# Kernel tuning notes

Measured on AMD Instinct MI355X. Metric: run time of the kernel, lower is better.

## Reference

```python
import jax, jax.numpy as jnp
import numpy as np

B, L, D, Y = 8, 2500, 512, 8921

def setup_inputs() -> dict:
    key = jax.random.key(0)
    k1, k2, k3, k4 = jax.random.split(key, 4)
    x = jax.random.normal(k1, (B, L, D), dtype=jnp.float32)
    # xavier-ish init scale for the label-attention and output matrices
    scale = (2.0 / (Y + D)) ** 0.5
    U_w = jax.random.normal(k2, (Y, D), dtype=jnp.float32) * scale
    final_w = jax.random.normal(k3, (Y, D), dtype=jnp.float32) * scale
    final_b = jax.random.normal(k4, (Y,), dtype=jnp.float32) * 0.01
    return {"x": x, "U_w": U_w, "final_w": final_w, "final_b": final_b}

def reference(x, U_w, final_w, final_b):
    # scores[b, y, l] = U_w[y, :] . x[b, l, :]
    scores = jnp.einsum('yd,bld->byl', U_w, x)            # (B, Y, L)
    alpha = jax.nn.softmax(scores, axis=2)                 # softmax over seq dim
    m = jnp.einsum('byl,bld->byd', alpha, x)               # (B, Y, D)
    y = jnp.einsum('yd,byd->by', final_w, m) + final_b     # (B, Y)
    return y
```

## Files before the change

kernel.cpp:

```cpp
#include <hip/hip_runtime.h>
#include <hip/hip_bf16.h>

#define NB 8
#define NL 2500
#define ND 512
#define NY 8921

#define BM 256
#define BN 256
#define BK 32
#define NKS 16
#define LPAD 2560
#define NLT 10
#define NYB 70
#define YPAD 8960

#define SPLIT 5
#define LSPL_MAIN 2

#define TILE 16384
#define GT_BYTES ((size_t)NYB * NKS * TILE)
#define XT_BYTES ((size_t)NB * NLT * NKS * TILE)
#define P_ELEMS  ((size_t)SPLIT * NB * YPAD)
#define P_BYTES  (P_ELEMS * 4)

typedef short s8v __attribute__((ext_vector_type(8)));
typedef float f4v __attribute__((ext_vector_type(4)));

__device__ __forceinline__ unsigned short f2bf(float f) {
  unsigned int u = __float_as_uint(f);
  return (unsigned short)((u + 0x7FFFu + ((u >> 16) & 1u)) >> 16);
}
__device__ __forceinline__ unsigned int pk2(float a, float b) {
  return (unsigned int)f2bf(a) | ((unsigned int)f2bf(b) << 16);
}
__device__ __forceinline__ void async_copy16(const char* g, char* l) {
  __builtin_amdgcn_global_load_lds(
      (const __attribute__((address_space(1))) void*)g,
      (__attribute__((address_space(3))) void*)l, 16, 0, 0);
}

__device__ __forceinline__ int tile_off(int r, int gn) {
  int rp = r >> 1;
  return rp * 128 + ((((r & 1) << 6) | (gn << 4)) ^ ((rp & 7) << 4));
}

__global__ void cvt_g_kernel(const float* __restrict__ U, const float* __restrict__ W,
                             char* __restrict__ Gt) {
  int c = blockIdx.x * 256 + threadIdx.x;
  int g10 = c & 1023;
  int tile = c >> 10;
  int ks = tile & 15, yblk = tile >> 4;
  int r = g10 >> 2, gn = g10 & 3;
  int rg = yblk * 256 + r;
  int y = rg >> 1;
  uint4 o;
  if (y < NY) {
    const float* src = (rg & 1) ? W : U;
    const float4* p = (const float4*)(src + (size_t)y * ND + ks * BK + gn * 8);
    float4 f0 = p[0], f1 = p[1];
    o.x = pk2(f0.x, f0.y); o.y = pk2(f0.z, f0.w);
    o.z = pk2(f1.x, f1.y); o.w = pk2(f1.z, f1.w);
  } else {
    o = make_uint4(0u, 0u, 0u, 0u);
  }
  *(uint4*)(Gt + (size_t)tile * TILE + tile_off(r, gn)) = o;
}

__global__ void cvt_x_kernel(const float* __restrict__ x, char* __restrict__ Xt) {
  int c = blockIdx.x * 256 + threadIdx.x;
  int g10 = c & 1023;
  int tile = c >> 10;
  int ks = tile & 15, rest = tile >> 4;
  int t = rest % NLT, b = rest / NLT;
  int r = g10 >> 2, gn = g10 & 3;
  int l = t * 256 + r;
  uint4 o;
  if (l < NL) {
    const float4* p = (const float4*)(x + ((size_t)b * NL + l) * ND + ks * BK + gn * 8);
    float4 f0 = p[0], f1 = p[1];
    o.x = pk2(f0.x, f0.y); o.y = pk2(f0.z, f0.w);
    o.z = pk2(f1.x, f1.y); o.w = pk2(f1.z, f1.w);
  } else {
    o = make_uint4(0u, 0u, 0u, 0u);
  }
  *(uint4*)(Xt + (size_t)tile * TILE + tile_off(r, gn)) = o;
}

template<int LSPL, int NSPL, bool PARTIAL>
__global__ __launch_bounds__(512, 2) void fused_kernel(
    const char* __restrict__ Gt, const char* __restrict__ Xt,
    const float* __restrict__ bias, float* __restrict__ out,
    float* __restrict__ PD, float* __restrict__ PN)
{
  __shared__ uint4 ring[8192];
  char* ringC = (char*)ring;

  constexpr int NS = LSPL * NKS;

  const int tid  = threadIdx.x;
  const int lane = tid & 63;
  const int w    = tid >> 6;
  const int wr   = w >> 2;
  const int wc   = w & 3;
  const int cl   = lane & 15, g = lane >> 4;

  const int id    = blockIdx.x;
  const int bb    = id & 7;
  const int n     = id >> 3;
  const int yblk  = n / NSPL;
  const int split = n - yblk * NSPL;
  const int tbase = split * LSPL;

  const char* GA = Gt + (size_t)yblk * NKS * TILE;
  const char* XB = Xt + ((size_t)bb * NLT + tbase) * NKS * TILE;

  f4v acc[8][4];
  float runD[8][2], runN[8][2];
  #pragma unroll
  for (int mi = 0; mi < 8; ++mi)
    #pragma unroll
    for (int p = 0; p < 2; ++p) { runD[mi][p] = 0.f; runN[mi][p] = 0.f; }

  int aoff[8], boff[4];
  #pragma unroll
  for (int j = 0; j < 8; ++j) aoff[j] = tile_off(wr * 128 + j * 16 + cl, g);
  #pragma unroll
  for (int ni = 0; ni < 4; ++ni) boff[ni] = tile_off(wc * 64 + ni * 16 + cl, g);

  const int t16 = tid << 4;
  auto stageA = [&](int s) {
    const char* ga = GA + (size_t)(s & 15) * TILE;
    char* la = ringC + (s & 3) * TILE + (w << 10);
    async_copy16(ga + t16, la);
    async_copy16(ga + 8192 + t16, la + 8192);
  };
  auto stageB = [&](int s) {
    const char* gb = XB + (size_t)s * TILE;
    char* lb = ringC + 65536 + (s & 3) * TILE + (w << 10);
    async_copy16(gb + t16, lb);
    async_copy16(gb + 8192 + t16, lb + 8192);
  };

  stageA(0); stageB(0);
  stageA(1); stageB(1);
  stageA(2); stageB(2);
  asm volatile("s_waitcnt vmcnt(4)" ::: "memory");
  __builtin_amdgcn_s_barrier();
  asm volatile("" ::: "memory");

  s8v bvA[4], afA[4], bvB[4], afB[4], a47[4];
  {
    const char* A0 = ringC;
    const char* B0 = ringC + 65536;
    #pragma unroll
    for (int ni = 0; ni < 4; ++ni) bvA[ni] = *(const s8v*)(B0 + boff[ni]);
    #pragma unroll
    for (int j = 0; j < 4; ++j)    afA[j] = *(const s8v*)(A0 + aoff[j]);
  }

#define K_STEP(U, CBV, CAF, NBV, NAF)                                          \
  do {                                                                         \
    const int u_  = (U);                                                       \
    const int ks_ = u_ & (NKS - 1);                                            \
    const char* A_ = ringC + (u_ & 3) * TILE;                                  \
    if (ks_ == 0) {                                                            \
      _Pragma("unroll")                                                        \
      for (int mi = 0; mi < 8; ++mi)                                           \
        _Pragma("unroll")                                                      \
        for (int ni = 0; ni < 4; ++ni)                                         \
          _Pragma("unroll")                                                    \
          for (int q = 0; q < 4; ++q) acc[mi][ni][q] = 0.f;                    \
    }                                                                          \
    if (u_ + 3 < NS) { stageA(u_ + 3); stageB(u_ + 3); }                       \
    _Pragma("unroll")                                                          \
    for (int j = 0; j < 4; ++j) a47[j] = *(const s8v*)(A_ + aoff[4 + j]);      \
    __builtin_amdgcn_sched_barrier(0);                                         \
    __builtin_amdgcn_s_setprio(1);                                             \
    _Pragma("unroll")                                                          \
    for (int j = 0; j < 4; ++j)                                                \
      _Pragma("unroll")                                                        \
      for (int ni = 0; ni < 4; ++ni)                                           \
        acc[j][ni] = __builtin_amdgcn_mfma_f32_16x16x32_bf16(                  \
            CAF[j], CBV[ni], acc[j][ni], 0, 0, 0);                             \
    __builtin_amdgcn_s_setprio(0);                                             \
    __builtin_amdgcn_sched_barrier(0);                                         \
    if (u_ + 1 < NS) {                                                         \
      const char* An_ = ringC + ((u_ + 1) & 3) * TILE;                         \
      const char* Bn_ = ringC + 65536 + ((u_ + 1) & 3) * TILE;                 \
      _Pragma("unroll")                                                        \
      for (int ni = 0; ni < 4; ++ni) NBV[ni] = *(const s8v*)(Bn_ + boff[ni]);  \
      _Pragma("unroll")                                                        \
      for (int j = 0; j < 4; ++j)    NAF[j] = *(const s8v*)(An_ + aoff[j]);    \
    }                                                                          \
    __builtin_amdgcn_sched_barrier(0);                                         \
    __builtin_amdgcn_s_setprio(1);                                             \
    _Pragma("unroll")                                                          \
    for (int j = 0; j < 4; ++j)                                                \
      _Pragma("unroll")                                                        \
      for (int ni = 0; ni < 4; ++ni)                                           \
        acc[4 + j][ni] = __builtin_amdgcn_mfma_f32_16x16x32_bf16(              \
            a47[j], CBV[ni], acc[4 + j][ni], 0, 0, 0);                         \
    __builtin_amdgcn_s_setprio(0);                                             \
    if (ks_ == NKS - 1) {                                                      \
      const int lbase = (tbase + (u_ >> 4)) * BN + wc * 64 + cl;               \
      _Pragma("unroll")                                                        \
      for (int mi = 0; mi < 8; ++mi) {                                         \
        _Pragma("unroll")                                                      \
        for (int p = 0; p < 2; ++p) {                                          \
          float se = 0.f, ste = 0.f;                                           \
          _Pragma("unroll")                                                    \
          for (int ni = 0; ni < 4; ++ni) {                                     \
            bool valid = (lbase + ni * 16) < NL;                               \
            float sv = valid ? acc[mi][ni][2 * p] : -1e30f;                    \
            float e = __expf(sv);                                              \
            se += e;                                                           \
            ste += e * acc[mi][ni][2 * p + 1];                                 \
          }                                                                    \
          runD[mi][p] += se;                                                   \
          runN[mi][p] += ste;                                                  \
        }                                                                      \
      }                                                                        \
    }                                                                          \
    if (u_ <= NS - 4) {                                                        \
      asm volatile("s_waitcnt vmcnt(4)" ::: "memory");                         \
    } else if (u_ == NS - 3) {                                                 \
      asm volatile("s_waitcnt vmcnt(0)" ::: "memory");                         \
    }                                                                          \
    __builtin_amdgcn_s_barrier();                                              \
    asm volatile("" ::: "memory");                                             \
  } while (0)

  for (int uu = 0; uu < NS; uu += 2) {
    K_STEP(uu,     bvA, afA, bvB, afB);
    K_STEP(uu + 1, bvB, afB, bvA, afA);
  }
#undef K_STEP

  #pragma unroll
  for (int mi = 0; mi < 8; ++mi)
    #pragma unroll
    for (int p = 0; p < 2; ++p) {
      float d = runD[mi][p], nn = runN[mi][p];
      #pragma unroll
      for (int off = 1; off < 16; off <<= 1) {
        d += __shfl_xor(d, off);
        nn += __shfl_xor(nn, off);
      }
      runD[mi][p] = d; runN[mi][p] = nn;
    }

  __syncthreads();
  float* sm = (float*)ring;
  if (cl == 0) {
    #pragma unroll
    for (int mi = 0; mi < 8; ++mi)
      #pragma unroll
      for (int p = 0; p < 2; ++p) {
        int lab = wr * 64 + mi * 8 + 2 * g + p;
        float* s2 = sm + (lab * 4 + wc) * 2;
        s2[0] = runD[mi][p]; s2[1] = runN[mi][p];
      }
  }
  __syncthreads();
  if (tid < 128) {
    float D = 0.f, N = 0.f;
    #pragma unroll
    for (int q = 0; q < 4; ++q) {
      const float* s2 = sm + (tid * 4 + q) * 2;
      D += s2[0]; N += s2[1];
    }
    int y = yblk * 128 + tid;
    if constexpr (PARTIAL) {
      size_t o = ((size_t)split * NB + bb) * YPAD + y;
      PD[o] = D; PN[o] = N;
    } else {
      if (y < NY) out[(size_t)bb * NY + y] = N / D + bias[y];
    }
  }
}

__global__ void merge_kernel(const float* __restrict__ PD, const float* __restrict__ PN,
                             const float* __restrict__ bias, float* __restrict__ out) {
  int idx = blockIdx.x * 256 + threadIdx.x;
  int b = idx / YPAD, y = idx - b * YPAD;
  if (y >= NY) return;
  float D = 0.f, N = 0.f;
  #pragma unroll
  for (int s = 0; s < SPLIT; ++s) {
    size_t o = ((size_t)s * NB + b) * YPAD + y;
    D += PD[o];
    N += PN[o];
  }
  out[(size_t)b * NY + y] = N / D + bias[y];
}

extern "C" void kernel_launch(void* const* d_in, const int* in_sizes, int n_in,
                              void* d_out, int out_size, void* d_ws, size_t ws_size,
                              hipStream_t stream) {
  const float* xf   = (const float*)d_in[0];
  const float* Uf   = (const float*)d_in[1];
  const float* Wf   = (const float*)d_in[2];
  const float* bias = (const float*)d_in[3];
  float* out = (float*)d_out;

  char* Gt = (char*)d_ws;
  char* Xt = Gt + GT_BYTES;
  float* PD = (float*)(Xt + XT_BYTES);
  float* PN = PD + P_ELEMS;

  cvt_g_kernel<<<4480, 256, 0, stream>>>(Uf, Wf, Gt);
  cvt_x_kernel<<<5120, 256, 0, stream>>>(xf, Xt);

  const size_t need_main = GT_BYTES + XT_BYTES + 2 * P_BYTES;
  if (ws_size >= need_main) {
    fused_kernel<LSPL_MAIN, SPLIT, true><<<NYB * NB * SPLIT, 512, 0, stream>>>(
        Gt, Xt, bias, out, PD, PN);
    merge_kernel<<<NB * YPAD / 256, 256, 0, stream>>>(PD, PN, bias, out);
  } else {
    fused_kernel<NLT, 1, false><<<NYB * NB, 512, 0, stream>>>(
        Gt, Xt, bias, out, PD, PN);
  }
}
```

Baseline: 375.6 us.

## Load X fragments directly from global and shrink LDS ring to double buffer

The X conversion kernel now writes a fragment-major layout, so each wave can load its MFMA B fragments straight from global memory into registers instead of staging them through LDS. The LDS ring is cut from four A+B stages (128KB) to two A-only stages (32KB). The prefetch distance drops to one step with a full vmcnt(0) wait each iteration, and A fragments are read from LDS within the step rather than prefetched. The smaller LDS footprint may allow more blocks per CU. The cost is shallower latency hiding, and each B fragment is now fetched from global by two waves instead of once per block.

```diff
diff --git a/kernel.cpp b/kernel.cpp
--- a/kernel.cpp
+++ b/kernel.cpp
@@ -19,8 +19,9 @@
 #define LSPL_MAIN 2
 
 #define TILE 16384
+#define XSTEP 16384
 #define GT_BYTES ((size_t)NYB * NKS * TILE)
-#define XT_BYTES ((size_t)NB * NLT * NKS * TILE)
+#define XT_BYTES ((size_t)NB * NLT * NKS * XSTEP)
 #define P_ELEMS  ((size_t)SPLIT * NB * YPAD)
 #define P_BYTES  (P_ELEMS * 4)
 
@@ -69,22 +70,22 @@
 
 __global__ void cvt_x_kernel(const float* __restrict__ x, char* __restrict__ Xt) {
   int c = blockIdx.x * 256 + threadIdx.x;
-  int g10 = c & 1023;
-  int tile = c >> 10;
-  int ks = tile & 15, rest = tile >> 4;
-  int t = rest % NLT, b = rest / NLT;
-  int r = g10 >> 2, gn = g10 & 3;
+  int r  = c & 255;
+  int g  = (c >> 8) & 3;
+  int ks = (c >> 10) & 15;
+  int bt = c >> 14;
+  int t = bt % NLT, b = bt / NLT;
   int l = t * 256 + r;
   uint4 o;
   if (l < NL) {
-    const float4* p = (const float4*)(x + ((size_t)b * NL + l) * ND + ks * BK + gn * 8);
+    const float4* p = (const float4*)(x + ((size_t)b * NL + l) * ND + ks * BK + g * 8);
     float4 f0 = p[0], f1 = p[1];
     o.x = pk2(f0.x, f0.y); o.y = pk2(f0.z, f0.w);
     o.z = pk2(f1.x, f1.y); o.w = pk2(f1.z, f1.w);
   } else {
     o = make_uint4(0u, 0u, 0u, 0u);
   }
-  *(uint4*)(Xt + (size_t)tile * TILE + tile_off(r, gn)) = o;
+  *(uint4*)(Xt + (size_t)c * 16) = o;
 }
 
 template<int LSPL, int NSPL, bool PARTIAL>
@@ -93,7 +94,7 @@
     const float* __restrict__ bias, float* __restrict__ out,
     float* __restrict__ PD, float* __restrict__ PN)
 {
-  __shared__ uint4 ring[8192];
+  __shared__ uint4 ring[2048];
   char* ringC = (char*)ring;
 
   constexpr int NS = LSPL * NKS;
@@ -103,7 +104,7 @@
   const int w    = tid >> 6;
   const int wr   = w >> 2;
   const int wc   = w & 3;
-  const int cl   = lane & 15, g = lane >> 4;
+  const int cl   = lane & 15, g4 = lane >> 4;
 
   const int id    = blockIdx.x;
   const int bb    = id & 7;
@@ -113,7 +114,7 @@
   const int tbase = split * LSPL;
 
   const char* GA = Gt + (size_t)yblk * NKS * TILE;
-  const char* XB = Xt + ((size_t)bb * NLT + tbase) * NKS * TILE;
+  const char* XB = Xt + (size_t)(bb * NLT + tbase) * NKS * XSTEP;
 
   f4v acc[8][4];
   float runD[8][2], runN[8][2];
@@ -122,48 +123,56 @@
     #pragma unroll
     for (int p = 0; p < 2; ++p) { runD[mi][p] = 0.f; runN[mi][p] = 0.f; }
 
-  int aoff[8], boff[4];
+  int aoff[8];
   #pragma unroll
-  for (int j = 0; j < 8; ++j) aoff[j] = tile_off(wr * 128 + j * 16 + cl, g);
-  #pragma unroll
-  for (int ni = 0; ni < 4; ++ni) boff[ni] = tile_off(wc * 64 + ni * 16 + cl, g);
+  for (int j = 0; j < 8; ++j) aoff[j] = tile_off(wr * 128 + j * 16 + cl, g4);
+  const int boffg = g4 * 4096 + (wc * 64 + cl) * 16;
 
   const int t16 = tid << 4;
   auto stageA = [&](int s) {
     const char* ga = GA + (size_t)(s & 15) * TILE;
-    char* la = ringC + (s & 3) * TILE + (w << 10);
+    char* la = ringC + (s & 1) * TILE + (w << 10);
     async_copy16(ga + t16, la);
     async_copy16(ga + 8192 + t16, la + 8192);
   };
-  auto stageB = [&](int s) {
-    const char* gb = XB + (size_t)s * TILE;
-    char* lb = ringC + 65536 + (s & 3) * TILE + (w << 10);
-    async_copy16(gb + t16, lb);
-    async_copy16(gb + 8192 + t16, lb + 8192);
+
+  auto softmax_acc = [&](int tt) {
+    const int lbase = (tbase + tt) * BN + wc * 64 + cl;
+    #pragma unroll
+    for (int mi = 0; mi < 8; ++mi) {
+      #pragma unroll
+      for (int p = 0; p < 2; ++p) {
+        float se = 0.f, ste = 0.f;
+        #pragma unroll
+        for (int ni = 0; ni < 4; ++ni) {
+          bool valid = (lbase + ni * 16) < NL;
+          float sv = valid ? acc[mi][ni][2 * p] : -1e30f;
+          float e = __expf(sv);
+          se += e;
+          ste += e * acc[mi][ni][2 * p + 1];
+        }
+        runD[mi][p] += se;
+        runN[mi][p] += ste;
+      }
+    }
   };
 
-  stageA(0); stageB(0);
-  stageA(1); stageB(1);
-  stageA(2); stageB(2);
-  asm volatile("s_waitcnt vmcnt(4)" ::: "memory");
+  s8v bvA[4], bvB[4];
+  stageA(0);
+  {
+    const char* bsrc = XB + boffg;
+    #pragma unroll
+    for (int ni = 0; ni < 4; ++ni) bvA[ni] = *(const s8v*)(bsrc + ni * 256);
+  }
+  asm volatile("s_waitcnt vmcnt(0)" ::: "memory");
   __builtin_amdgcn_s_barrier();
   asm volatile("" ::: "memory");
 
-  s8v bvA[4], afA[4], bvB[4], afB[4], a47[4];
-  {
-    const char* A0 = ringC;
-    const char* B0 = ringC + 65536;
-    #pragma unroll
-    for (int ni = 0; ni < 4; ++ni) bvA[ni] = *(const s8v*)(B0 + boff[ni]);
-    #pragma unroll
-    for (int j = 0; j < 4; ++j)    afA[j] = *(const s8v*)(A0 + aoff[j]);
-  }
-
-#define K_STEP(U, CBV, CAF, NBV, NAF)                                          \
+#define K_STEP(U, BVC, BVN)                                                    \
   do {                                                                         \
     const int u_  = (U);                                                       \
     const int ks_ = u_ & (NKS - 1);                                            \
-    const char* A_ = ringC + (u_ & 3) * TILE;                                  \
+    const char* A_ = ringC + (u_ & 1) * TILE;                                  \
     if (ks_ == 0) {                                                            \
       _Pragma("unroll")                                                        \
       for (int mi = 0; mi < 8; ++mi)                                           \
@@ -172,68 +181,45 @@
           _Pragma("unroll")                                                    \
           for (int q = 0; q < 4; ++q) acc[mi][ni][q] = 0.f;                    \
     }                                                                          \
-    if (u_ + 3 < NS) { stageA(u_ + 3); stageB(u_ + 3); }                       \
+    if (u_ + 1 < NS) {                                                         \
+      stageA(u_ + 1);                                                          \
+      const int un_ = u_ + 1;                                                  \
+      const char* bsrc_ = XB + (size_t)(un_ >> 4) * (NKS * XSTEP)              \
+                        + (size_t)(un_ & 15) * XSTEP + boffg;                  \
+      _Pragma("unroll")                                                        \
+      for (int ni = 0; ni < 4; ++ni) BVN[ni] = *(const s8v*)(bsrc_ + ni * 256);\
+    }                                                                          \
+    __builtin_amdgcn_sched_barrier(0);     \
+    s8v af03[4], af47[4];                                                      \
     _Pragma("unroll")                                                          \
-    for (int j = 0; j < 4; ++j) a47[j] = *(const s8v*)(A_ + aoff[4 + j]);      \
-    __builtin_amdgcn_sched_barrier(0);                                         \
+    for (int j = 0; j < 4; ++j) af03[j] = *(const s8v*)(A_ + aoff[j]);         \
     __builtin_amdgcn_s_setprio(1);                                             \
     _Pragma("unroll")                                                          \
     for (int j = 0; j < 4; ++j)                                                \
       _Pragma("unroll")                                                        \
       for (int ni = 0; ni < 4; ++ni)                                           \
         acc[j][ni] = __builtin_amdgcn_mfma_f32_16x16x32_bf16(                  \
-            CAF[j], CBV[ni], acc[j][ni], 0, 0, 0);                             \
+            af03[j], BVC[ni], acc[j][ni], 0, 0, 0);                            \
     __builtin_amdgcn_s_setprio(0);                                             \
-    __builtin_amdgcn_sched_barrier(0);                                         \
-    if (u_ + 1 < NS) {                                                         \
-      const char* An_ = ringC + ((u_ + 1) & 3) * TILE;                         \
-      const char* Bn_ = ringC + 65536 + ((u_ + 1) & 3) * TILE;                 \
-      _Pragma("unroll")                                                        \
-      for (int ni = 0; ni < 4; ++ni) NBV[ni] = *(const s8v*)(Bn_ + boff[ni]);  \
-      _Pragma("unroll")                                                        \
-      for (int j = 0; j < 4; ++j)    NAF[j] = *(const s8v*)(An_ + aoff[j]);    \
-    }                                                                          \
-    __builtin_amdgcn_sched_barrier(0);                                         \
+    _Pragma("unroll")                                                          \
+    for (int j = 0; j < 4; ++j) af47[j] = *(const s8v*)(A_ + aoff[4 + j]);     \
     __builtin_amdgcn_s_setprio(1);                                             \
     _Pragma("unroll")                                                          \
     for (int j = 0; j < 4; ++j)                                                \
       _Pragma("unroll")                                                        \
       for (int ni = 0; ni < 4; ++ni)                                           \
         acc[4 + j][ni] = __builtin_amdgcn_mfma_f32_16x16x32_bf16(              \
-            a47[j], CBV[ni], acc[4 + j][ni], 0, 0, 0);                         \
+            af47[j], BVC[ni], acc[4 + j][ni], 0, 0, 0);                        \
     __builtin_amdgcn_s_setprio(0);                                             \
-    if (ks_ == NKS - 1) {                                                      \
-      const int lbase = (tbase + (u_ >> 4)) * BN + wc * 64 + cl;               \
-      _Pragma("unroll")                                                        \
-      for (int mi = 0; mi < 8; ++mi) {                                         \
-        _Pragma("unroll")                                                      \
-        for (int p = 0; p < 2; ++p) {                                          \
-          float se = 0.f, ste = 0.f;                                           \
-          _Pragma("unroll")                                                    \
-          for (int ni = 0; ni < 4; ++ni) {                                     \
-            bool valid = (lbase + ni * 16) < NL;                               \
-            float sv = valid ? acc[mi][ni][2 * p] : -1e30f;                    \
-            float e = __expf(sv);                                              \
-            se += e;                                                           \
-            ste += e * acc[mi][ni][2 * p + 1];                                 \
-          }                                                                    \
-          runD[mi][p] += se;                                                   \
-          runN[mi][p] += ste;                                                  \
-        }                                                                      \
-      }                                                                        \
-    }                                                                          \
-    if (u_ <= NS - 4) {                                                        \
-      asm volatile("s_waitcnt vmcnt(4)" ::: "memory");                         \
-    } else if (u_ == NS - 3) {                                                 \
-      asm volatile("s_waitcnt vmcnt(0)" ::: "memory");                         \
-    }                                                                          \
+    if (ks_ == NKS - 1) softmax_acc(u_ >> 4);                                  \
+    asm volatile("s_waitcnt vmcnt(0)" ::: "memory");                           \
     __builtin_amdgcn_s_barrier();                                              \
     asm volatile("" ::: "memory");                                             \
   } while (0)
 
   for (int uu = 0; uu < NS; uu += 2) {
-    K_STEP(uu,     bvA, afA, bvB, afB);
-    K_STEP(uu + 1, bvB, afB, bvA, afA);
+    K_STEP(uu,     bvA, bvB);
+    K_STEP(uu + 1, bvB, bvA);
   }
 #undef K_STEP
 
@@ -257,7 +243,7 @@
     for (int mi = 0; mi < 8; ++mi)
       #pragma unroll
       for (int p = 0; p < 2; ++p) {
-        int lab = wr * 64 + mi * 8 + 2 * g + p;
+        int lab = wr * 64 + mi * 8 + 2 * g4 + p;
         float* s2 = sm + (lab * 4 + wc) * 2;
         s2[0] = runD[mi][p]; s2[1] = runN[mi][p];
       }
```

New measurement: 430.8 us. 1.15x slower.
